# Kernel tuning notes

Hardware: AMD Instinct MI355X
Metric: run time of the kernel (lower is better)

## Reference

```python
import jax, jax.numpy as jnp
import numpy as np

H = 1024

def setup_inputs() -> dict:
    key = jax.random.key(0)
    ks = jax.random.split(key, 10)
    B, S = 4, 2048
    hidden_states = jax.random.normal(ks[0], (B, S, H), dtype=jnp.float32)
    attention_mask = jnp.zeros((B, S, S), dtype=jnp.float32)
    prosody_mask = jax.random.uniform(ks[1], (B, S, S), dtype=jnp.float32)
    sc = 1.0 / np.sqrt(H)
    Wq = jax.random.normal(ks[2], (H, H), dtype=jnp.float32) * sc
    bq = jnp.zeros((H,), dtype=jnp.float32)
    Wk = jax.random.normal(ks[3], (H, H), dtype=jnp.float32) * sc
    bk = jnp.zeros((H,), dtype=jnp.float32)
    Wv = jax.random.normal(ks[4], (H, H), dtype=jnp.float32) * sc
    bv = jnp.zeros((H,), dtype=jnp.float32)
    prosody_weight = jax.random.normal(ks[5], (1,), dtype=jnp.float32)
    return {"hidden_states": hidden_states, "attention_mask": attention_mask,
            "prosody_mask": prosody_mask, "Wq": Wq, "bq": bq, "Wk": Wk, "bk": bk,
            "Wv": Wv, "bv": bv, "prosody_weight": prosody_weight}

def reference(hidden_states, attention_mask, prosody_mask, Wq, bq, Wk, bk, Wv, bv, prosody_weight):
    # q,k,v: [B,S,H]; torch Linear is x @ W.T + b
    q = jnp.einsum('bsh,oh->bso', hidden_states, Wq) + bq
    k = jnp.einsum('bsh,oh->bso', hidden_states, Wk) + bk
    v = jnp.einsum('bsh,oh->bso', hidden_states, Wv) + bv
    scale = 1.0 / jnp.sqrt(jnp.float32(hidden_states.shape[-1]))
    scores = jnp.einsum('bqh,bkh->bqk', q, k) * scale  # [B,S,S]
    scores = scores + attention_mask + prosody_weight[0] * prosody_mask
    probs = jax.nn.softmax(scores, axis=-1)
    context = jnp.einsum('bqk,bkh->bqh', probs, v)
    return context
```

## Files before the change

### kernel.cpp

```cpp
#include <hip/hip_runtime.h>
#include <hip/hip_bf16.h>
#include <stdint.h>

typedef unsigned short u16;
typedef __attribute__((ext_vector_type(8))) __bf16 bf16x8;
typedef __attribute__((ext_vector_type(4))) float f32x4;
typedef __attribute__((ext_vector_type(8))) u16 u16x8;
typedef __attribute__((ext_vector_type(4))) u16 u16x4;

typedef const __attribute__((address_space(1))) void GV;
typedef __attribute__((address_space(3))) void LV;

__device__ __forceinline__ u16 f2bf(float f) {
  union { float f; uint32_t u; } c; c.f = f;
  uint32_t u = c.u;
  u = u + 0x7FFFu + ((u >> 16) & 1u);
  return (u16)(u >> 16);
}

#define BM 128
#define BN 128
#define BK 32

template<int MODE>
__global__ __launch_bounds__(256) void gemm_bt(
    const u16* __restrict__ A, const u16* __restrict__ B,
    int K, int lda, int ldb,
    long sAb, long sBb,
    float* __restrict__ Cf, int ldc, long sCb,
    u16* __restrict__ Qo, u16* __restrict__ Ko, u16* __restrict__ Vo,
    const float* __restrict__ bias)
{
  const int tid = threadIdx.x;
  const int lane = tid & 63;
  const int w = tid >> 6;
  const int wr = w >> 1, wc = w & 1;
  const int bz = blockIdx.z;
  const u16* Ab = A + (long)bz * sAb;
  const u16* Bb = B + (long)bz * sBb;
  const int row0 = blockIdx.y * BM;
  const int col0 = blockIdx.x * BN;

  __shared__ u16 As[BM][BK];
  __shared__ u16 Bs[BN][BK];

  f32x4 acc[4][4];
#pragma unroll
  for (int i = 0; i < 4; ++i)
#pragma unroll
    for (int j = 0; j < 4; ++j) acc[i][j] = (f32x4)(0.f);

  const int srow = w * 16 + (lane >> 2);
  const int scol = (lane & 3) * 8;
  const int fr = lane & 15;
  const int kq = (lane >> 4) * 8;

  const int nkt = K / BK;
  for (int kt = 0; kt < nkt; ++kt) {
    const int kb = kt * BK;
    __syncthreads();
#pragma unroll
    for (int j = 0; j < 2; ++j) {
      const u16* g = Ab + (long)(row0 + srow + j * 64) * lda + (kb + scol);
      __builtin_amdgcn_global_load_lds((GV*)g, (LV*)(&As[w * 16 + j * 64][0]), 16, 0, 0);
    }
#pragma unroll
    for (int j = 0; j < 2; ++j) {
      const u16* g = Bb + (long)(col0 + srow + j * 64) * ldb + (kb + scol);
      __builtin_amdgcn_global_load_lds((GV*)g, (LV*)(&Bs[w * 16 + j * 64][0]), 16, 0, 0);
    }
    asm volatile("s_waitcnt vmcnt(0)" ::: "memory");
    __syncthreads();

    bf16x8 af[4], bfr[4];
#pragma unroll
    for (int mi = 0; mi < 4; ++mi)
      af[mi] = *(const bf16x8*)(&As[wr * 64 + mi * 16 + fr][kq]);
#pragma unroll
    for (int ni = 0; ni < 4; ++ni)
      bfr[ni] = *(const bf16x8*)(&Bs[wc * 64 + ni * 16 + fr][kq]);
#pragma unroll
    for (int mi = 0; mi < 4; ++mi)
#pragma unroll
      for (int ni = 0; ni < 4; ++ni)
        acc[mi][ni] = __builtin_amdgcn_mfma_f32_16x16x32_bf16(af[mi], bfr[ni], acc[mi][ni], 0, 0, 0);
  }

  const int cr = (lane >> 4) * 4;
  const int cc = lane & 15;
#pragma unroll
  for (int mi = 0; mi < 4; ++mi) {
#pragma unroll
    for (int ni = 0; ni < 4; ++ni) {
      const int gcol = col0 + wc * 64 + ni * 16 + cc;
#pragma unroll
      for (int r = 0; r < 4; ++r) {
        const int grow = row0 + wr * 64 + mi * 16 + cr + r;
        float v = acc[mi][ni][r];
        if (MODE == 0) {
          Cf[(long)bz * sCb + (long)grow * ldc + gcol] = v;
        } else {
          v += bias[gcol];
          u16 h = f2bf(v);
          if (gcol < 1024)      Qo[(long)grow * 1024 + gcol] = h;
          else if (gcol < 2048) Ko[(long)grow * 1024 + (gcol - 1024)] = h;
          else                  Vo[(long)grow * 1024 + (gcol - 2048)] = h;
        }
      }
    }
  }
}

__global__ __launch_bounds__(256) void f32_to_bf16_vec(const float* __restrict__ in,
                                                       u16* __restrict__ o, long n)
{
  long i = ((long)blockIdx.x * 256 + threadIdx.x) * 4;
  if (i < n) {
    float4 v = *(const float4*)(in + i);
    u16x4 r; r[0] = f2bf(v.x); r[1] = f2bf(v.y); r[2] = f2bf(v.z); r[3] = f2bf(v.w);
    *(u16x4*)(o + i) = r;
  }
}

__global__ void concat_bias(const float* __restrict__ bq, const float* __restrict__ bk,
                            const float* __restrict__ bv, float* __restrict__ b)
{
  int i = blockIdx.x * 256 + threadIdx.x;
  if (i < 1024)      b[i] = bq[i];
  else if (i < 2048) b[i] = bk[i - 1024];
  else if (i < 3072) b[i] = bv[i - 2048];
}

__global__ __launch_bounds__(256) void transpose_bf16(const u16* __restrict__ V,
                                                      u16* __restrict__ Vt)
{
  __shared__ u16 t[32][33];
  const int b = blockIdx.z;
  const u16* Vb = V + (long)b * 2097152;
  u16* Vtb = Vt + (long)b * 2097152;
  const int tx = threadIdx.x & 31, ty = threadIdx.x >> 5;
  const int h0 = blockIdx.x * 32, s0 = blockIdx.y * 32;
#pragma unroll
  for (int i = 0; i < 4; ++i)
    t[ty + i * 8][tx] = Vb[(long)(s0 + ty + i * 8) * 1024 + h0 + tx];
  __syncthreads();
#pragma unroll
  for (int i = 0; i < 4; ++i)
    Vtb[(long)(h0 + ty + i * 8) * 2048 + s0 + tx] = t[tx][ty + i * 8];
}

__global__ __launch_bounds__(256) void softmax_rows(
    const float* scores, const float* __restrict__ am,
    const float* __restrict__ pm, const float* __restrict__ pw, u16* P)
{
  const long g = blockIdx.x;
  const int tid = threadIdx.x;
  const int lane = tid & 63;
  const int wv = tid >> 6;
  const float* s = scores + g * 2048;
  const float* a = am + g * 2048;
  const float* p = pm + g * 2048;
  u16* po = (u16*)((char*)P + g * 8192);
  const float wgt = pw[0];

  float sv[8], av[8], pvv[8], v[8];
  *(float4*)&sv[0]  = *(const float4*)(s + tid * 8);
  *(float4*)&sv[4]  = *(const float4*)(s + tid * 8 + 4);
  *(float4*)&av[0]  = *(const float4*)(a + tid * 8);
  *(float4*)&av[4]  = *(const float4*)(a + tid * 8 + 4);
  *(float4*)&pvv[0] = *(const float4*)(p + tid * 8);
  *(float4*)&pvv[4] = *(const float4*)(p + tid * 8 + 4);

  float mx = -3.0e38f;
#pragma unroll
  for (int i = 0; i < 8; ++i) {
    v[i] = fmaf(sv[i], 0.03125f, fmaf(wgt, pvv[i], av[i]));
    mx = fmaxf(mx, v[i]);
  }
#pragma unroll
  for (int off = 32; off >= 1; off >>= 1) mx = fmaxf(mx, __shfl_xor(mx, off, 64));
  __shared__ float rmax[4], rsum[4];
  if (lane == 0) rmax[wv] = mx;
  __syncthreads();
  mx = fmaxf(fmaxf(rmax[0], rmax[1]), fmaxf(rmax[2], rmax[3]));

  float sum = 0.f;
#pragma unroll
  for (int i = 0; i < 8; ++i) { v[i] = __expf(v[i] - mx); sum += v[i]; }
#pragma unroll
  for (int off = 32; off >= 1; off >>= 1) sum += __shfl_xor(sum, off, 64);
  if (lane == 0) rsum[wv] = sum;
  __syncthreads();
  sum = rsum[0] + rsum[1] + rsum[2] + rsum[3];
  const float inv = 1.0f / sum;

  u16x8 o;
#pragma unroll
  for (int i = 0; i < 8; ++i) o[i] = f2bf(v[i] * inv);
  *(u16x8*)(po + tid * 8) = o;
}

extern "C" void kernel_launch(void* const* d_in, const int* in_sizes, int n_in,
                              void* d_out, int out_size, void* d_ws, size_t ws_size,
                              hipStream_t stream) {
  const float* hs = (const float*)d_in[0];
  const float* am = (const float*)d_in[1];
  const float* pm = (const float*)d_in[2];
  const float* Wq = (const float*)d_in[3];
  const float* bq = (const float*)d_in[4];
  const float* Wk = (const float*)d_in[5];
  const float* bk = (const float*)d_in[6];
  const float* Wv = (const float*)d_in[7];
  const float* bv = (const float*)d_in[8];
  const float* pw = (const float*)d_in[9];
  float* out = (float*)d_out;

  char* w = (char*)d_ws;
  u16* X      = (u16*)(w);
  u16* Wqkv   = (u16*)(w + 16777216);
  float* bias = (float*)(w + 23068672);
  u16* Qb     = (u16*)(w + 23085056);
  u16* Kb     = (u16*)(w + 39862272);
  u16* Vb     = (u16*)(w + 56639488);
  float* sc   = (float*)(w + 73416704);
  u16* Vt     = X;
  u16* P      = (u16*)sc;

  hipLaunchKernelGGL(f32_to_bf16_vec, dim3(8192), dim3(256), 0, stream, hs, X, 8388608L);
  hipLaunchKernelGGL(f32_to_bf16_vec, dim3(1024), dim3(256), 0, stream, Wq, Wqkv, 1048576L);
  hipLaunchKernelGGL(f32_to_bf16_vec, dim3(1024), dim3(256), 0, stream, Wk, Wqkv + 1048576, 1048576L);
  hipLaunchKernelGGL(f32_to_bf16_vec, dim3(1024), dim3(256), 0, stream, Wv, Wqkv + 2097152, 1048576L);
  hipLaunchKernelGGL(concat_bias, dim3(12), dim3(256), 0, stream, bq, bk, bv, bias);

  hipLaunchKernelGGL((gemm_bt<1>), dim3(24, 64, 1), dim3(256), 0, stream,
                     X, Wqkv, 1024, 1024, 1024, 0L, 0L,
                     (float*)nullptr, 0, 0L, Qb, Kb, Vb, bias);

  hipLaunchKernelGGL(transpose_bf16, dim3(32, 64, 4), dim3(256), 0, stream, Vb, Vt);

  hipLaunchKernelGGL((gemm_bt<0>), dim3(16, 16, 4), dim3(256), 0, stream,
                     Qb, Kb, 1024, 1024, 1024, 2097152L, 2097152L,
                     sc, 2048, 4194304L,
                     (u16*)nullptr, (u16*)nullptr, (u16*)nullptr, (const float*)nullptr);

  hipLaunchKernelGGL(softmax_rows, dim3(8192), dim3(256), 0, stream, sc, am, pm, pw, P);

  hipLaunchKernelGGL((gemm_bt<0>), dim3(8, 16, 4), dim3(256), 0, stream,
                     P, Vt, 2048, 4096, 2048, 8388608L, 2097152L,
                     out, 1024, 2097152L,
                     (u16*)nullptr, (u16*)nullptr, (u16*)nullptr, (const float*)nullptr);
}
```

Measured before the change: 403.1 us.

## Double-buffer GEMM LDS tiles, swizzle LDS layout, and remap workgroups across XCDs

The GEMM kernel now keeps two LDS buffers, so the global-to-LDS load of the next K tile is issued before the MFMA work on the current tile, with a single wait and barrier per iteration. The LDS column slots are XOR-swizzled on both the write and read side to reduce bank conflicts on fragment reads. Workgroup IDs are also remapped so that contiguous output tiles land on the same XCD chiplet for better L2 reuse. This doubles LDS use per block and could cut occupancy. The remap assumes the tile count divides evenly by 8.

After: 379.8 us. 5.8% less time.

```diff
diff --git a/kernel.cpp b/kernel.cpp
--- a/kernel.cpp
+++ b/kernel.cpp
@@ -36,13 +36,21 @@
   const int w = tid >> 6;
   const int wr = w >> 1, wc = w & 1;
   const int bz = blockIdx.z;
+
+  const int nwg = gridDim.x * gridDim.y;
+  const int wg  = blockIdx.y * gridDim.x + blockIdx.x;
+  const int cpx = nwg >> 3;
+  const int swg = (wg & 7) * cpx + (wg >> 3);
+  const int bx  = swg % gridDim.x;
+  const int by  = swg / gridDim.x;
+
   const u16* Ab = A + (long)bz * sAb;
   const u16* Bb = B + (long)bz * sBb;
-  const int row0 = blockIdx.y * BM;
-  const int col0 = blockIdx.x * BN;
-
-  __shared__ u16 As[BM][BK];
-  __shared__ u16 Bs[BN][BK];
+  const int row0 = by * BM;
+  const int col0 = bx * BN;
+
+  __shared__ u16 As[2][BM][BK];
+  __shared__ u16 Bs[2][BN][BK];
 
   f32x4 acc[4][4];
 #pragma unroll
@@ -51,39 +59,61 @@
     for (int j = 0; j < 4; ++j) acc[i][j] = (f32x4)(0.f);
 
   const int srow = w * 16 + (lane >> 2);
-  const int scol = (lane & 3) * 8;
+  const int ssw  = (lane >> 3) & 3;
+  const int scol = (((lane & 3) ^ ssw) * 8);
   const int fr = lane & 15;
-  const int kq = (lane >> 4) * 8;
+  const int swr = (fr >> 1) & 3;
+  const int rslot = ((lane >> 4) ^ swr) * 8;
 
   const int nkt = K / BK;
+
+  {
+#pragma unroll
+    for (int j = 0; j < 2; ++j) {
+      const u16* g = Ab + (long)(row0 + srow + j * 64) * lda + scol;
+      __builtin_amdgcn_global_load_lds((GV*)g, (LV*)(&As[0][w * 16 + j * 64][0]), 16, 0, 0);
+    }
+#pragma unroll
+    for (int j = 0; j < 2; ++j) {
+      const u16* g = Bb + (long)(col0 + srow + j * 64) * ldb + scol;
+      __builtin_amdgcn_global_load_lds((GV*)g, (LV*)(&Bs[0][w * 16 + j * 64][0]), 16, 0, 0);
+    }
+  }
+  asm volatile("s_waitcnt vmcnt(0)" ::: "memory");
+  __syncthreads();
+
+  int cur = 0;
   for (int kt = 0; kt < nkt; ++kt) {
-    const int kb = kt * BK;
-    __syncthreads();
-#pragma unroll
-    for (int j = 0; j < 2; ++j) {
-      const u16* g = Ab + (long)(row0 + srow + j * 64) * lda + (kb + scol);
-      __builtin_amdgcn_global_load_lds((GV*)g, (LV*)(&As[w * 16 + j * 64][0]), 16, 0, 0);
-    }
-#pragma unroll
-    for (int j = 0; j < 2; ++j) {
-      const u16* g = Bb + (long)(col0 + srow + j * 64) * ldb + (kb + scol);
-      __builtin_amdgcn_global_load_lds((GV*)g, (LV*)(&Bs[w * 16 + j * 64][0]), 16, 0, 0);
-    }
+    if (kt + 1 < nkt) {
+      const int kb = (kt + 1) * BK;
+#pragma unroll
+      for (int j = 0; j < 2; ++j) {
+        const u16* g = Ab + (long)(row0 + srow + j * 64) * lda + (kb + scol);
+        __builtin_amdgcn_global_load_lds((GV*)g, (LV*)(&As[cur ^ 1][w * 16 + j * 64][0]), 16, 0, 0);
+      }
+#pragma unroll
+      for (int j = 0; j < 2; ++j) {
+        const u16* g = Bb + (long)(col0 + srow + j * 64) * ldb + (kb + scol);
+        __builtin_amdgcn_global_load_lds((GV*)g, (LV*)(&Bs[cur ^ 1][w * 16 + j * 64][0]), 16, 0, 0);
+      }
+    }
+
+    bf16x8 af[4], bfr[4];
+#pragma unroll
+    for (int mi = 0; mi < 4; ++mi)
+      af[mi] = *(const bf16x8*)(&As[cur][wr * 64 + mi * 16 + fr][rslot]);
+#pragma unroll
+    for (int ni = 0; ni < 4; ++ni)
+      bfr[ni] = *(const bf16x8*)(&Bs[cur][wc * 64 + ni * 16 + fr][rslot]);
+#pragma unroll
+    for (int mi = 0; mi < 4; ++mi)
+#pragma unroll
+      for (int ni = 0; ni < 4; ++ni)
+        acc[mi][ni] = __builtin_amdgcn_mfma_f32_16x16x32_bf16(af[mi], bfr[ni], acc[mi][ni], 0, 0, 0);
+
     asm volatile("s_waitcnt vmcnt(0)" ::: "memory");
     __syncthreads();
-
-    bf16x8 af[4], bfr[4];
-#pragma unroll
-    for (int mi = 0; mi < 4; ++mi)
-      af[mi] = *(const bf16x8*)(&As[wr * 64 + mi * 16 + fr][kq]);
-#pragma unroll
-    for (int ni = 0; ni < 4; ++ni)
-      bfr[ni] = *(const bf16x8*)(&Bs[wc * 64 + ni * 16 + fr][kq]);
-#pragma unroll
-    for (int mi = 0; mi < 4; ++mi)
-#pragma unroll
-      for (int ni = 0; ni < 4; ++ni)
-        acc[mi][ni] = __builtin_amdgcn_mfma_f32_16x16x32_bf16(af[mi], bfr[ni], acc[mi][ni], 0, 0, 0);
+    cur ^= 1;
   }
 
   const int cr = (lane >> 4) * 4;
```

## Triple-buffer GEMM LDS loads with XOR swizzle and block-index remapping

Applied to the files above, without the earlier changes.

The shared GEMM kernel gets a 3-stage LDS ring, so global-to-LDS loads for tiles kt+1 and kt+2 are in flight while tile kt is computed. This replaces the per-iteration full vmcnt(0) wait and double barrier with a partial wait and a single barrier. LDS columns are XOR-swizzled to cut bank conflicts on fragment reads, and workgroup indices are remapped in groups of 8 to improve cache locality. It also raises wave priority around the MFMA block. The cost is three times the LDS per block, which may lower occupancy, and the remapping assumes the workgroup count divides evenly by 8.

New measurement: 388.6 us. 3.6% less time.

```diff
diff --git a/kernel.cpp b/kernel.cpp
--- a/kernel.cpp
+++ b/kernel.cpp
@@ -36,13 +36,21 @@
   const int w = tid >> 6;
   const int wr = w >> 1, wc = w & 1;
   const int bz = blockIdx.z;
+
+  const int nwg = gridDim.x * gridDim.y;
+  const int wg  = blockIdx.y * gridDim.x + blockIdx.x;
+  const int cpx = nwg >> 3;
+  const int swg = (wg & 7) * cpx + (wg >> 3);
+  const int bx  = swg % gridDim.x;
+  const int by  = swg / gridDim.x;
+
   const u16* Ab = A + (long)bz * sAb;
   const u16* Bb = B + (long)bz * sBb;
-  const int row0 = blockIdx.y * BM;
-  const int col0 = blockIdx.x * BN;
-
-  __shared__ u16 As[BM][BK];
-  __shared__ u16 Bs[BN][BK];
+  const int row0 = by * BM;
+  const int col0 = bx * BN;
+
+  __shared__ u16 As[3][BM][BK];
+  __shared__ u16 Bs[3][BN][BK];
 
   f32x4 acc[4][4];
 #pragma unroll
@@ -51,39 +59,59 @@
     for (int j = 0; j < 4; ++j) acc[i][j] = (f32x4)(0.f);
 
   const int srow = w * 16 + (lane >> 2);
-  const int scol = (lane & 3) * 8;
+  const int ssw  = (lane >> 3) & 3;
+  const int scol = (((lane & 3) ^ ssw) * 8);
   const int fr = lane & 15;
-  const int kq = (lane >> 4) * 8;
+  const int swr = (fr >> 1) & 3;
+  const int rslot = ((lane >> 4) ^ swr) * 8;
 
   const int nkt = K / BK;
-  for (int kt = 0; kt < nkt; ++kt) {
+
+  auto STAGE = [&](int buf, int kt) {
     const int kb = kt * BK;
-    __syncthreads();
 #pragma unroll
     for (int j = 0; j < 2; ++j) {
       const u16* g = Ab + (long)(row0 + srow + j * 64) * lda + (kb + scol);
-      __builtin_amdgcn_global_load_lds((GV*)g, (LV*)(&As[w * 16 + j * 64][0]), 16, 0, 0);
+      __builtin_amdgcn_global_load_lds((GV*)g, (LV*)(&As[buf][w * 16 + j * 64][0]), 16, 0, 0);
     }
 #pragma unroll
     for (int j = 0; j < 2; ++j) {
       const u16* g = Bb + (long)(col0 + srow + j * 64) * ldb + (kb + scol);
-      __builtin_amdgcn_global_load_lds((GV*)g, (LV*)(&Bs[w * 16 + j * 64][0]), 16, 0, 0);
-    }
-    asm volatile("s_waitcnt vmcnt(0)" ::: "memory");
-    __syncthreads();
-
+      __builtin_amdgcn_global_load_lds((GV*)g, (LV*)(&Bs[buf][w * 16 + j * 64][0]), 16, 0, 0);
+    }
+  };
+
+  STAGE(0, 0);
+  if (nkt > 1) STAGE(1, 1);
+
+  for (int kt = 0; kt < nkt; ++kt) {
+    __builtin_amdgcn_sched_barrier(0);
+    if (kt < nkt - 1) {
+      asm volatile("s_waitcnt vmcnt(4)" ::: "memory");
+    } else {
+      asm volatile("s_waitcnt vmcnt(0)" ::: "memory");
+    }
+    __builtin_amdgcn_s_barrier();
+    __builtin_amdgcn_sched_barrier(0);
+
+    if (kt + 2 < nkt) STAGE((kt + 2) % 3, kt + 2);
+
+    const int cb = kt % 3;
     bf16x8 af[4], bfr[4];
 #pragma unroll
     for (int mi = 0; mi < 4; ++mi)
-      af[mi] = *(const bf16x8*)(&As[wr * 64 + mi * 16 + fr][kq]);
+      af[mi] = *(const bf16x8*)(&As[cb][wr * 64 + mi * 16 + fr][rslot]);
 #pragma unroll
     for (int ni = 0; ni < 4; ++ni)
-      bfr[ni] = *(const bf16x8*)(&Bs[wc * 64 + ni * 16 + fr][kq]);
+      bfr[ni] = *(const bf16x8*)(&Bs[cb][wc * 64 + ni * 16 + fr][rslot]);
+
+    __builtin_amdgcn_s_setprio(1);
 #pragma unroll
     for (int mi = 0; mi < 4; ++mi)
 #pragma unroll
       for (int ni = 0; ni < 4; ++ni)
         acc[mi][ni] = __builtin_amdgcn_mfma_f32_16x16x32_bf16(af[mi], bfr[ni], acc[mi][ni], 0, 0, 0);
+    __builtin_amdgcn_s_setprio(0);
   }
 
   const int cr = (lane >> 4) * 4;
```
